# Kernel tuning notes

Hardware: AMD Instinct MI355X
Metric: run time of the kernel (lower is better)

## Reference

```python
import jax, jax.numpy as jnp
import numpy as np

N_CELLS = 50000


def setup_inputs() -> dict:
    key = jax.random.key(0)
    ks = jax.random.split(key, 8)
    in_dim, emb = 1000, 128
    sl0 = 1.0 / np.sqrt(in_dim)
    sl1 = 1.0 / np.sqrt(emb)
    return {
        "x": jax.random.normal(ks[0], (in_dim, N_CELLS), dtype=jnp.float32),
        "knn_edge_index": jax.random.randint(ks[1], (2, 800000), 0, N_CELLS, dtype=jnp.int64),
        "W_l0": jax.random.normal(ks[2], (emb, in_dim), dtype=jnp.float32) * sl0,
        "b_l0": jnp.zeros((emb,), dtype=jnp.float32),
        "W_r0": jax.random.normal(ks[3], (emb, in_dim), dtype=jnp.float32) * sl0,
        "W_l1": jax.random.normal(ks[4], (emb, emb), dtype=jnp.float32) * sl1,
        "b_l1": jnp.zeros((emb,), dtype=jnp.float32),
        "W_r1": jax.random.normal(ks[5], (emb, emb), dtype=jnp.float32) * sl1,
    }


def _sage_layer(h, src, dst, W_l, b_l, W_r, n_nodes):
    # mean aggregation of source-node features onto target nodes (PyG SAGEConv default)
    agg = jax.ops.segment_sum(h[src], dst, num_segments=n_nodes)      # [N, d_in]
    cnt = jax.ops.segment_sum(jnp.ones((src.shape[0],), h.dtype), dst,
                              num_segments=n_nodes)                   # [N]
    mean_nbr = agg / jnp.maximum(cnt, 1.0)[:, None]
    out = mean_nbr @ W_l.T + b_l + h @ W_r.T                          # [N, d_out]
    return jax.nn.elu(out)  # dropout is identity in eval mode


def reference(x, knn_edge_index, W_l0, b_l0, W_r0, W_l1, b_l1, W_r1):
    src, dst = knn_edge_index[0], knn_edge_index[1]
    h = x.T                                            # (num_cells, num_genes)
    n = h.shape[0]
    h = _sage_layer(h, src, dst, W_l0, b_l0, W_r0, n)
    h = _sage_layer(h, src, dst, W_l1, b_l1, W_r1, n)
    return h
```

## Files before the change

kernel.cpp:

```cpp
#include <hip/hip_runtime.h>
#include <hip/hip_bf16.h>


#define IN_DIM 1000

#define KBARRIER() asm volatile("s_waitcnt lgkmcnt(0)\n\ts_barrier" ::: "memory")

typedef __attribute__((ext_vector_type(8))) short bf16x8;
typedef __attribute__((ext_vector_type(4))) float f32x4;

static __device__ __forceinline__ unsigned int f2bf(float f){
  union { float f; unsigned int u; } v; v.f = f;
  return (v.u + 0x7fffu + ((v.u >> 16) & 1u)) >> 16;
}
static __device__ __forceinline__ float bl(unsigned v){
  union { unsigned u; float f; } t; t.u = v << 16; return t.f;
}
static __device__ __forceinline__ float bh(unsigned v){
  union { unsigned u; float f; } t; t.u = v & 0xFFFF0000u; return t.f;
}
static __device__ __forceinline__ void glds16(const void* g, void* lds){
  __builtin_amdgcn_global_load_lds(
      (const __attribute__((address_space(1))) unsigned int*)g,
      (__attribute__((address_space(3))) unsigned int*)lds, 16, 0, 0);
}

__global__ void prep_k(const float* __restrict__ Wl0, const float* __restrict__ Wr0,
                       const float* __restrict__ Wl1, const float* __restrict__ Wr1,
                       unsigned short* __restrict__ img0,
                       unsigned short* __restrict__ img1, int total0, int total1,
                       int* __restrict__ zptr, int zn){
  int idx = blockIdx.x*256 + threadIdx.x;
  if (idx < total0){
    int j  = idx & 7;
    int l  = (idx >> 3) & 63;
    int ks = (idx >> 9) & 1;
    int n  = (idx >> 10) & 3;
    int w  = (idx >> 12) & 3;
    int s  = idx >> 14;
    int row = w*64 + n*16 + (l & 15);
    int k   = s*64 + ks*32 + (l >> 4)*8 + j;
    float val = 0.f;
    if (k < IN_DIM)
      val = (row < 128) ? Wl0[(size_t)row*IN_DIM + k] : Wr0[(size_t)(row-128)*IN_DIM + k];
    img0[idx] = (unsigned short)f2bf(val);
    return;
  }
  idx -= total0;
  if (idx < total1){
    int s   = idx / (256*72);
    int rem = idx % (256*72);
    int n   = rem / 72;
    int e   = rem % 72;
    float val = 0.f;
    if (e < 64){
      int k = s*64 + e;
      if (k < 128) val = (n < 128) ? Wl1[(size_t)n*128 + k] : Wr1[(size_t)(n-128)*128 + k];
    }
    img1[idx] = (unsigned short)f2bf(val);
    return;
  }
  idx -= total1;
  if (idx < zn) zptr[idx] = 0;
}

__global__ void scan1_k(const int* __restrict__ cnt, int* __restrict__ rowp,
                        float* __restrict__ inv, int* __restrict__ bsum,
                        int* __restrict__ ticket, int N, int nb){
  __shared__ int wt[4];
  __shared__ int lastS;
  int bid = blockIdx.x;
  int i = bid*256 + threadIdx.x;
  int lane = threadIdx.x & 63, wid = threadIdx.x >> 6;
  int v = (i < N) ? cnt[i] : 0;
  int sc = v;
  #pragma unroll
  for (int off = 1; off < 64; off <<= 1){
    int o = __shfl_up(sc, off);
    if (lane >= off) sc += o;
  }
  if (lane == 63) wt[wid] = sc;
  __syncthreads();
  if (threadIdx.x == 0){
    int a = 0;
    #pragma unroll
    for (int j = 0; j < 4; ++j){ int t = wt[j]; wt[j] = a; a += t; }
    bsum[bid] = a;
    if (bid == nb-1 && (N & 255)) rowp[N] = a;
  }
  __syncthreads();
  if (i < N){
    rowp[i] = wt[wid] + sc - v;
    inv[i]  = 1.0f / fmaxf((float)v, 1.0f);
  }
  __threadfence();
  if (threadIdx.x == 0){
    int t = __hip_atomic_fetch_add(ticket, 1, __ATOMIC_ACQ_REL, __HIP_MEMORY_SCOPE_AGENT);
    lastS = (t == (int)gridDim.x - 1);
  }
  __syncthreads();
  if (lastS){
    __threadfence();
    int t2 = threadIdx.x;
    int bv = (t2 < nb) ? __hip_atomic_load(&bsum[t2], __ATOMIC_RELAXED,
                                           __HIP_MEMORY_SCOPE_AGENT) : 0;
    int sc2 = bv;
    #pragma unroll
    for (int off = 1; off < 64; off <<= 1){
      int o = __shfl_up(sc2, off);
      if (lane >= off) sc2 += o;
    }
    __syncthreads();
    if (lane == 63) wt[wid] = sc2;
    __syncthreads();
    if (t2 == 0){
      int a = 0;
      #pragma unroll
      for (int j = 0; j < 4; ++j){ int t = wt[j]; wt[j] = a; a += t; }
      bsum[nb] = a;
      if (!(N & 255)) rowp[N] = 0;
    }
    __syncthreads();
    if (t2 < nb) bsum[t2] = wt[wid] + sc2 - bv;
  }
}

__global__ void fill_col_k(const int* __restrict__ ei, int E,
                           const int* __restrict__ rowp, const int* __restrict__ bsum,
                           int* __restrict__ pos, int* __restrict__ col){
  int e = blockIdx.x*blockDim.x + threadIdx.x;
  if (e < E){
    int src = ei[e];
    int dst = ei[(size_t)E + e];
    int p = atomicAdd(&pos[dst], 1);
    col[rowp[dst] + bsum[dst >> 8] + p] = src;
  }
}

__global__ __launch_bounds__(256, 2) void gemm0_count_k(
    const float* __restrict__ x, const unsigned short* __restrict__ B0img,
    unsigned short* __restrict__ ybl, unsigned short* __restrict__ ybr,
    int N, int Ka, int nsteps, int nblk,
    const int* __restrict__ ei, int E, int* __restrict__ cnt){
  if ((int)blockIdx.x >= nblk){
    int idx = ((int)blockIdx.x - nblk)*256 + threadIdx.x;
    if (idx < E) atomicAdd(&cnt[ei[(size_t)E + idx]], 1);
    return;
  }
  __shared__ char AsB[128*144];
  const int tid = threadIdx.x;
  const int c0  = blockIdx.x * 128;
  const int l   = tid & 63, wid = tid >> 6;
  const int nw  = wid * 64;
  const int lr  = l & 15, lq = l >> 4;
  const int c4  = (tid & 31)*4;
  const int kg  = tid >> 5;
  const int ce  = c0 + c4;
  const int ceff = (ce < N) ? ce : 0;

  f32x4 acc[8][4];
  #pragma unroll
  for (int m=0;m<8;++m)
    #pragma unroll
    for (int n=0;n<4;++n) acc[m][n] = (f32x4){0.f,0.f,0.f,0.f};

  const char* bbase = (const char*)B0img + (size_t)wid*8192 + (size_t)l*16;

  float2 xv0[8], xv1[8];
  bf16x8 bf[8];

  auto loadx = [&](int step){
    #pragma unroll
    for (int kk = 0; kk < 8; ++kk){
      int k = step*64 + kg*8 + kk;
      k = (k < Ka) ? k : (Ka - 1);
      const float* p = &x[(size_t)k*N + ceff];
      xv0[kk] = *(const float2*)p;
      xv1[kk] = *(const float2*)(p + 2);
    }
  };
  auto loadB = [&](int s){
    const char* p = bbase + (size_t)s*32768;
    #pragma unroll
    for (int n = 0; n < 4; ++n)
      #pragma unroll
      for (int ks = 0; ks < 2; ++ks)
        bf[n*2+ks] = *(const bf16x8*)(p + n*2048 + ks*1024);
  };
  auto packx = [&](){
    unsigned w0[4], w1[4], w2[4], w3[4];
    #pragma unroll
    for (int j = 0; j < 4; ++j){
      asm("v_cvt_pk_bf16_f32 %0, %1, %2" : "=v"(w0[j]) : "v"(xv0[2*j].x), "v"(xv0[2*j+1].x));
      asm("v_cvt_pk_bf16_f32 %0, %1, %2" : "=v"(w1[j]) : "v"(xv0[2*j].y), "v"(xv0[2*j+1].y));
      asm("v_cvt_pk_bf16_f32 %0, %1, %2" : "=v"(w2[j]) : "v"(xv1[2*j].x), "v"(xv1[2*j+1].x));
      asm("v_cvt_pk_bf16_f32 %0, %1, %2" : "=v"(w3[j]) : "v"(xv1[2*j].y), "v"(xv1[2*j+1].y));
    }
    *(uint4*)&AsB[(c4+0)*144 + kg*16] = make_uint4(w0[0],w0[1],w0[2],w0[3]);
    *(uint4*)&AsB[(c4+1)*144 + kg*16] = make_uint4(w1[0],w1[1],w1[2],w1[3]);
    *(uint4*)&AsB[(c4+2)*144 + kg*16] = make_uint4(w2[0],w2[1],w2[2],w2[3]);
    *(uint4*)&AsB[(c4+3)*144 + kg*16] = make_uint4(w3[0],w3[1],w3[2],w3[3]);
  };
  auto domfma = [&](){
    #pragma unroll
    for (int ks = 0; ks < 2; ++ks){
      bf16x8 a[8];
      #pragma unroll
      for (int m = 0; m < 8; ++m)
        a[m] = *(const bf16x8*)&AsB[(m*16 + lr)*144 + ks*64 + lq*16];
      #pragma unroll
      for (int n = 0; n < 4; ++n)
        #pragma unroll
        for (int m = 0; m < 8; ++m)
          acc[m][n] = __builtin_amdgcn_mfma_f32_16x16x32_bf16(a[m], bf[n*2+ks], acc[m][n], 0, 0, 0);
    }
  };

  loadx(0);
  for (int s = 0; s < nsteps; ++s){
    if (s) KBARRIER();
    loadB(s);
    packx();
    if (s + 1 < nsteps) loadx(s + 1);
    KBARRIER();
    domfma();
  }

  unsigned short* op = (nw < 128) ? ybl : ybr;
  const int       nc = (nw < 128) ? nw : nw - 128;
  #pragma unroll
  for (int m = 0; m < 8; ++m){
    int rbase = c0 + m*16 + lq*4;
    #pragma unroll
    for (int q = 0; q < 4; ++q){
      int r2 = rbase + q;
      if (r2 < N){
        #pragma unroll
        for (int n = 0; n < 4; ++n)
          op[(size_t)r2*128 + nc + n*16 + lr] = (unsigned short)f2bf(acc[m][n][q]);
      }
    }
  }
}

__global__ __launch_bounds__(256, 2) void gemm1_k(
    const void* __restrict__ Ap, const unsigned short* __restrict__ Bimg,
    unsigned short* __restrict__ ybl, unsigned short* __restrict__ ybr,
    int N, int nsteps){
  __shared__ char AsB[128*128];
  __shared__ char BsB[36864];
  const int tid = threadIdx.x;
  const int c0  = blockIdx.x * 128;
  const int l   = tid & 63, wid = tid >> 6;
  const int nw  = wid * 64;
  const int lr  = l & 15, lq = l >> 4;

  f32x4 acc[8][4];
  #pragma unroll
  for (int m=0;m<8;++m)
    #pragma unroll
    for (int n=0;n<4;++n) acc[m][n] = (f32x4){0.f,0.f,0.f,0.f};

  const char* h1b = (const char*)Ap;

  for (int s = 0; s < nsteps; ++s){
    if (s) __syncthreads();
    {
      const char* bsrc = (const char*)Bimg + (size_t)s*36864;
      #pragma unroll
      for (int i = 0; i < 9; ++i){
        int chunk = i*256 + tid;
        glds16(bsrc + (size_t)chunk*16, &BsB[(i*256 + wid*64)*16]);
      }
    }
    #pragma unroll
    for (int i = 0; i < 4; ++i){
      int chunk = i*256 + tid;
      int row = chunk >> 3, cb = (chunk & 7)*16;
      glds16(h1b + (size_t)(c0 + row)*256 + s*128 + cb,
             &AsB[(i*256 + wid*64)*16]);
    }
    __syncthreads();
    #pragma unroll
    for (int ks = 0; ks < 2; ++ks){
      bf16x8 a[8];
      #pragma unroll
      for (int m = 0; m < 8; ++m){
        int row = m*16 + lr;
        int colb = (ks*64 + lq*16) ^ ((row & 7) << 4);
        a[m] = *(const bf16x8*)&AsB[row*128 + colb];
      }
      #pragma unroll
      for (int n = 0; n < 4; ++n){
        bf16x8 b = *(const bf16x8*)&BsB[(nw + n*16 + lr)*144 + ks*64 + lq*16];
        #pragma unroll
        for (int m = 0; m < 8; ++m)
          acc[m][n] = __builtin_amdgcn_mfma_f32_16x16x32_bf16(a[m], b, acc[m][n], 0, 0, 0);
      }
    }
  }
  unsigned short* op  = (nw < 128) ? ybl : ybr;
  const int       nc  = (nw < 128) ? nw : nw - 128;
  #pragma unroll
  for (int m = 0; m < 8; ++m){
    int rbase = c0 + m*16 + lq*4;
    #pragma unroll
    for (int q = 0; q < 4; ++q){
      int r = rbase + q;
      if (r < N){
        #pragma unroll
        for (int n = 0; n < 4; ++n)
          op[(size_t)r*128 + nc + n*16 + lr] = (unsigned short)f2bf(acc[m][n][q]);
      }
    }
  }
}

template<int LAYER>
__global__ void aggregate_k(const unsigned short* __restrict__ ybl,
    const unsigned short* __restrict__ ybr,
    const int* __restrict__ rowp, const int* __restrict__ bsum,
    const int* __restrict__ col,
    const float* __restrict__ inv, const float* __restrict__ bias,
    void* __restrict__ outp, int N){
  int node = blockIdx.x*4 + (threadIdx.x >> 6);
  int l = threadIdx.x & 63;
  if (node >= N) return;
  int b = rowp[node]   + bsum[node >> 8];
  int e = rowp[node+1] + bsum[(node+1) >> 8];
  int f2 = l*2;
  const unsigned* yl = (const unsigned*)ybl;
  float s0=0.f,s1=0.f,t0=0.f,t1=0.f,u0=0.f,u1=0.f,w0=0.f,w1=0.f;
  for (int kb = b; kb < e; kb += 64){
    int rem = e - kb; if (rem > 64) rem = 64;
    int myc = (l < rem) ? col[kb + l] : 0;
    for (int j = 0; j < rem; j += 16){
      unsigned a[16];
      #pragma unroll
      for (int jj = 0; jj < 16; ++jj){
        int src = __shfl(myc, j + jj);
        unsigned v = yl[(size_t)src*64 + l];
        a[jj] = (j + jj < rem) ? v : 0u;
      }
      #pragma unroll
      for (int h = 0; h < 2; ++h){
        s0 += bl(a[h*8+0]); s1 += bh(a[h*8+0]); t0 += bl(a[h*8+1]); t1 += bh(a[h*8+1]);
        u0 += bl(a[h*8+2]); u1 += bh(a[h*8+2]); w0 += bl(a[h*8+3]); w1 += bh(a[h*8+3]);
        s0 += bl(a[h*8+4]); s1 += bh(a[h*8+4]); t0 += bl(a[h*8+5]); t1 += bh(a[h*8+5]);
        u0 += bl(a[h*8+6]); u1 += bh(a[h*8+6]); w0 += bl(a[h*8+7]); w1 += bh(a[h*8+7]);
      }
    }
  }
  s0 = (s0 + t0) + (u0 + w0);
  s1 = (s1 + t1) + (u1 + w1);
  unsigned vs = *(const unsigned*)&ybr[(size_t)node*128 + f2];
  float iv = inv[node];
  float r0 = s0*iv + bias[f2]   + bl(vs);
  float r1 = s1*iv + bias[f2+1] + bh(vs);
  r0 = (r0 > 0.f) ? r0 : expm1f(r0);
  r1 = (r1 > 0.f) ? r1 : expm1f(r1);
  if (LAYER == 0){
    int sf = f2 >> 6, fo = f2 & 63, g = fo >> 3;
    size_t byte = (size_t)node*256 + (size_t)(sf*128 + ((g ^ (node & 7)) << 4) + (fo & 7)*2);
    *(unsigned*)((char*)outp + byte) = f2bf(r0) | (f2bf(r1) << 16);
  } else {
    *(float2*)((float*)outp + (size_t)node*128 + f2) = make_float2(r0, r1);
  }
}

static inline size_t align_up(size_t v, size_t a){ return (v + a - 1) & ~(a - 1); }

extern "C" void kernel_launch(void* const* d_in, const int* in_sizes, int n_in,
                              void* d_out, int out_size, void* d_ws, size_t ws_size,
                              hipStream_t stream) {
  const float* x   = (const float*)d_in[0];
  const int*   ei  = (const int*)d_in[1];
  const float* Wl0 = (const float*)d_in[2];
  const float* bl0 = (const float*)d_in[3];
  const float* Wr0 = (const float*)d_in[4];
  const float* Wl1 = (const float*)d_in[5];
  const float* bl1 = (const float*)d_in[6];
  const float* Wr1 = (const float*)d_in[7];

  int N = in_sizes[0] / IN_DIM;
  int E = in_sizes[1] / 2;

  const int NS0 = 16;
  const int NS1 = 2;
  int nsb = (N + 255) / 256;

  char* base = (char*)d_ws;
  size_t off = 0;
  unsigned short* ybl = (unsigned short*)(base + off); off = align_up(off + (size_t)N*128*2, 256);
  unsigned short* ybr = (unsigned short*)(base + off); off = align_up(off + (size_t)N*128*2, 256);
  float* inv  = (float*)(base + off); off = align_up(off + (size_t)N*4, 256);
  int*   cnt  = (int*)  (base + off); off = align_up(off + (size_t)N*8 + 256, 256);
  int*   pos  = cnt + N;
  int*   ticket = cnt + 2*N;
  int*   rowp = (int*)  (base + off); off = align_up(off + (size_t)(N+1)*4, 256);
  int*   bsum = (int*)  (base + off); off = align_up(off + (size_t)(nsb+1)*4, 256);
  int*   col  = (int*)  (base + off); off = align_up(off + (size_t)E*4, 256);
  unsigned short* B0img = (unsigned short*)(base + off); off = align_up(off + (size_t)524288*2, 256);
  unsigned short* B1img = (unsigned short*)(base + off); off = align_up(off + (size_t)NS1*18432*2, 256);
  void* h1b = d_out;
  (void)ws_size; (void)n_in; (void)out_size;

  int t0n = 524288, t1n = NS1*18432;
  int zn  = 2*N + 64;
  prep_k<<<(t0n+t1n+zn+255)/256, 256, 0, stream>>>(Wl0, Wr0, Wl1, Wr1,
                                                   B0img, B1img, t0n, t1n,
                                                   cnt, zn);

  int nblk = (N + 127) / 128;
  int cblk = (E + 255) / 256;
  int ablk = (N + 3) / 4;

  gemm0_count_k<<<nblk + cblk, 256, 0, stream>>>(x, B0img, ybl, ybr, N, IN_DIM,
                                                 NS0, nblk, ei, E, cnt);
  scan1_k<<<nsb, 256, 0, stream>>>(cnt, rowp, inv, bsum, ticket, N, nsb);
  fill_col_k<<<(E+255)/256, 256, 0, stream>>>(ei, E, rowp, bsum, pos, col);
  aggregate_k<0><<<ablk, 256, 0, stream>>>(ybl, ybr, rowp, bsum, col, inv, bl0, h1b, N);

  gemm1_k<<<nblk, 256, 0, stream>>>(h1b, B1img, ybl, ybr, N, NS1);
  aggregate_k<1><<<ablk, 256, 0, stream>>>(ybl, ybr, rowp, bsum, col, inv, bl1, d_out, N);
}
```

Baseline: 211.8 us.

## Pre-transpose x to bf16 cell-major and stream A tiles via global_load_lds

Adds a separate kernel that converts x from fp32 gene-major to a bf16 cell-major padded buffer. The first GEMM then loads A tiles directly into an XOR-swizzled LDS layout with global_load_lds, dropping the in-loop fp32 loads, conversion and register prefetch. This cuts GEMM register pressure and conversion work, but adds a full extra pass that reads x and writes a roughly 100MB bf16 copy. The register double-buffering of x is lost, so each step now waits on the LDS fill before the barrier.

```diff
diff --git a/kernel.cpp b/kernel.cpp
--- a/kernel.cpp
+++ b/kernel.cpp
@@ -3,8 +3,6 @@
 
 
 #define IN_DIM 1000
-
-#define KBARRIER() asm volatile("s_waitcnt lgkmcnt(0)\n\ts_barrier" ::: "memory")
 
 typedef __attribute__((ext_vector_type(8))) short bf16x8;
 typedef __attribute__((ext_vector_type(4))) float f32x4;
@@ -64,6 +62,38 @@
   if (idx < zn) zptr[idx] = 0;
 }
 
+__global__ void xconv_k(const float* __restrict__ x, unsigned short* __restrict__ xb,
+                        int N, int Ka){
+  __shared__ unsigned short t[64][80];
+  int bid = blockIdx.x;
+  int kt = bid & 15;
+  int ct = bid >> 4;
+  int k0 = kt*64, c0 = ct*64;
+  int tid = threadIdx.x;
+  int cl  = (tid & 15)*4;
+  int kl0 = tid >> 4;
+  #pragma unroll
+  for (int r = 0; r < 4; ++r){
+    int kl = r*16 + kl0;
+    int k  = k0 + kl;
+    int c  = c0 + cl;
+    float4 v = make_float4(0.f,0.f,0.f,0.f);
+    if (k < Ka && c < N) v = *(const float4*)&x[(size_t)k*N + c];
+    t[cl+0][kl] = (unsigned short)f2bf(v.x);
+    t[cl+1][kl] = (unsigned short)f2bf(v.y);
+    t[cl+2][kl] = (unsigned short)f2bf(v.z);
+    t[cl+3][kl] = (unsigned short)f2bf(v.w);
+  }
+  __syncthreads();
+  #pragma unroll
+  for (int it = 0; it < 2; ++it){
+    int u = it*256 + tid;
+    int cell = u >> 3, g = u & 7;
+    uint4 w = *(const uint4*)&t[cell][g*8];
+    *(uint4*)((char*)xb + (size_t)(c0 + cell)*2048 + (size_t)kt*128 + g*16) = w;
+  }
+}
+
 __global__ void scan1_k(const int* __restrict__ cnt, int* __restrict__ rowp,
                         float* __restrict__ inv, int* __restrict__ bsum,
                         int* __restrict__ ticket, int N, int nb){
@@ -138,25 +168,23 @@
 }
 
 __global__ __launch_bounds__(256, 2) void gemm0_count_k(
-    const float* __restrict__ x, const unsigned short* __restrict__ B0img,
+    const unsigned short* __restrict__ xb, const unsigned short* __restrict__ B0img,
     unsigned short* __restrict__ ybl, unsigned short* __restrict__ ybr,
-    int N, int Ka, int nsteps, int nblk,
+    int N, int nsteps, int nblk,
     const int* __restrict__ ei, int E, int* __restrict__ cnt){
   if ((int)blockIdx.x >= nblk){
     int idx = ((int)blockIdx.x - nblk)*256 + threadIdx.x;
     if (idx < E) atomicAdd(&cnt[ei[(size_t)E + idx]], 1);
     return;
   }
-  __shared__ char AsB[128*144];
+  __shared__ char AsB[128*128];
   const int tid = threadIdx.x;
   const int c0  = blockIdx.x * 128;
   const int l   = tid & 63, wid = tid >> 6;
   const int nw  = wid * 64;
   const int lr  = l & 15, lq = l >> 4;
-  const int c4  = (tid & 31)*4;
-  const int kg  = tid >> 5;
-  const int ce  = c0 + c4;
-  const int ceff = (ce < N) ? ce : 0;
+  const int arow  = l >> 3;
+  const int aslot = ((l & 7) ^ arow) << 4;
 
   f32x4 acc[8][4];
   #pragma unroll
@@ -165,20 +193,8 @@
     for (int n=0;n<4;++n) acc[m][n] = (f32x4){0.f,0.f,0.f,0.f};
 
   const char* bbase = (const char*)B0img + (size_t)wid*8192 + (size_t)l*16;
-
-  float2 xv0[8], xv1[8];
   bf16x8 bf[8];
 
-  auto loadx = [&](int step){
-    #pragma unroll
-    for (int kk = 0; kk < 8; ++kk){
-      int k = step*64 + kg*8 + kk;
-      k = (k < Ka) ? k : (Ka - 1);
-      const float* p = &x[(size_t)k*N + ceff];
-      xv0[kk] = *(const float2*)p;
-      xv1[kk] = *(const float2*)(p + 2);
-    }
-  };
   auto loadB = [&](int s){
     const char* p = bbase + (size_t)s*32768;
     #pragma unroll
@@ -187,27 +203,13 @@
       for (int ks = 0; ks < 2; ++ks)
         bf[n*2+ks] = *(const bf16x8*)(p + n*2048 + ks*1024);
   };
-  auto packx = [&](){
-    unsigned w0[4], w1[4], w2[4], w3[4];
-    #pragma unroll
-    for (int j = 0; j < 4; ++j){
-      asm("v_cvt_pk_bf16_f32 %0, %1, %2" : "=v"(w0[j]) : "v"(xv0[2*j].x), "v"(xv0[2*j+1].x));
-      asm("v_cvt_pk_bf16_f32 %0, %1, %2" : "=v"(w1[j]) : "v"(xv0[2*j].y), "v"(xv0[2*j+1].y));
-      asm("v_cvt_pk_bf16_f32 %0, %1, %2" : "=v"(w2[j]) : "v"(xv1[2*j].x), "v"(xv1[2*j+1].x));
-      asm("v_cvt_pk_bf16_f32 %0, %1, %2" : "=v"(w3[j]) : "v"(xv1[2*j].y), "v"(xv1[2*j+1].y));
-    }
-    *(uint4*)&AsB[(c4+0)*144 + kg*16] = make_uint4(w0[0],w0[1],w0[2],w0[3]);
-    *(uint4*)&AsB[(c4+1)*144 + kg*16] = make_uint4(w1[0],w1[1],w1[2],w1[3]);
-    *(uint4*)&AsB[(c4+2)*144 + kg*16] = make_uint4(w2[0],w2[1],w2[2],w2[3]);
-    *(uint4*)&AsB[(c4+3)*144 + kg*16] = make_uint4(w3[0],w3[1],w3[2],w3[3]);
-  };
   auto domfma = [&](){
     #pragma unroll
     for (int ks = 0; ks < 2; ++ks){
       bf16x8 a[8];
       #pragma unroll
       for (int m = 0; m < 8; ++m)
-        a[m] = *(const bf16x8*)&AsB[(m*16 + lr)*144 + ks*64 + lq*16];
+        a[m] = *(const bf16x8*)&AsB[(m*16 + lr)*128 + ((ks*64 + lq*16) ^ ((lr & 7) << 4))];
       #pragma unroll
       for (int n = 0; n < 4; ++n)
         #pragma unroll
@@ -216,13 +218,16 @@
     }
   };
 
-  loadx(0);
   for (int s = 0; s < nsteps; ++s){
-    if (s) KBARRIER();
+    if (s) __syncthreads();
+    #pragma unroll
+    for (int i = 0; i < 4; ++i){
+      int rbase = wid*32 + i*8;
+      glds16((const char*)xb + (size_t)(c0 + rbase + arow)*2048 + (size_t)s*128 + aslot,
+             &AsB[rbase*128]);
+    }
     loadB(s);
-    packx();
-    if (s + 1 < nsteps) loadx(s + 1);
-    KBARRIER();
+    __syncthreads();
     domfma();
   }
 
@@ -402,6 +407,7 @@
   int*   col  = (int*)  (base + off); off = align_up(off + (size_t)E*4, 256);
   unsigned short* B0img = (unsigned short*)(base + off); off = align_up(off + (size_t)524288*2, 256);
   unsigned short* B1img = (unsigned short*)(base + off); off = align_up(off + (size_t)NS1*18432*2, 256);
+  unsigned short* xb    = (unsigned short*)(base + off); off = align_up(off + (size_t)50176*1024*2, 256);
   void* h1b = d_out;
   (void)ws_size; (void)n_in; (void)out_size;
 
@@ -411,11 +417,14 @@
                                                    B0img, B1img, t0n, t1n,
                                                    cnt, zn);
 
+  int ctiles = (50176 + 63) / 64;
+  xconv_k<<<16*ctiles, 256, 0, stream>>>(x, xb, N, IN_DIM);
+
   int nblk = (N + 127) / 128;
   int cblk = (E + 255) / 256;
   int ablk = (N + 3) / 4;
 
-  gemm0_count_k<<<nblk + cblk, 256, 0, stream>>>(x, B0img, ybl, ybr, N, IN_DIM,
+  gemm0_count_k<<<nblk + cblk, 256, 0, stream>>>(xb, B0img, ybl, ybr, N,
                                                  NS0, nblk, ei, E, cnt);
   scan1_k<<<nsb, 256, 0, stream>>>(cnt, rowp, inv, bsum, ticket, N, nsb);
   fill_col_k<<<(E+255)/256, 256, 0, stream>>>(ei, E, rowp, bsum, pos, col);
```

New measurement: 257.2 us. 1.21x slower.
